# Optimization experiments

Measured on AMD Instinct MI355X. Metric: run time of the kernel, lower is better.

## Reference

```python
import jax, jax.numpy as jnp
import numpy as np
from math import pi

B, L, S, D, H, M, DK, IND, KS = 8, 3072, 3072, 512, 8, 2, 64, 96, 25


def _linear(x, W, b):
    return x @ W + b


def _moving_avg(x, k):
    # Autoformer-style moving average with edge replication, stride 1.  x: [B, T, D]
    pad = (k - 1) // 2
    xp = jnp.concatenate([jnp.repeat(x[:, :1], pad, axis=1), x,
                          jnp.repeat(x[:, -1:], pad, axis=1)], axis=1)
    c = jnp.cumsum(xp, axis=1)
    c = jnp.concatenate([jnp.zeros_like(c[:, :1]), c], axis=1)
    return (c[:, k:] - c[:, :-k]) / k


def _trend_norm(x, g, b):
    # series_decomp(kernel=25): LayerNorm the seasonal part, add back the trend.
    trend = _moving_avg(x, KS)
    seas = x - trend
    mu = jnp.mean(seas, axis=-1, keepdims=True)
    var = jnp.var(seas, axis=-1, keepdims=True)
    return (seas - mu) * jax.lax.rsqrt(var + 1e-5) * g + b + trend


def _quat_attention(q, k, v, q_om, q_th, k_om, k_th):
    # q: [B,Lq,H,E]; k,v: [B,Sk,H,E]; omegas/thetas: [B,*,H,M]
    Bq, Lq, Hh, E = q.shape
    Sk = k.shape[1]
    Mm = q_om.shape[-1]
    qpos = (jnp.arange(Lq, dtype=q.dtype) / Lq)[None, :, None, None]
    kpos = (jnp.arange(Sk, dtype=q.dtype) / Sk)[None, :, None, None]
    Qa = q_om * qpos + q_th
    Ka = k_om * kpos + k_th
    Qc, Qs = jnp.cos(Qa), jnp.sin(Qa)
    Kc, Ks = jnp.cos(Ka), jnp.sin(Ka)
    q0, q1, q2, q3 = jnp.split(q, 4, axis=-1)
    k0, k1, k2, k3 = jnp.split(k, 4, axis=-1)
    op = lambda a, t: jnp.einsum('blhe,blhm->blhme', a, t)
    Qr = jnp.concatenate([op(q0, Qc) - op(q1, Qs), op(q1, Qc) + op(q0, Qs),
                          op(q2, Qc) + op(q3, Qs), op(q3, Qc) - op(q2, Qs)], axis=-1)
    Kr = jnp.concatenate([op(k0, Kc) - op(k2, Ks), op(k1, Kc) - op(k3, Ks),
                          op(k2, Kc) + op(k0, Ks), op(k3, Kc) + op(k1, Ks)], axis=-1)
    scores = jnp.einsum('blhme,bshme->bhls', Qr, Kr) / Mm
    scale = 1.0 / jnp.sqrt(jnp.asarray(E, q.dtype))
    A = jax.nn.softmax(scale * scores, axis=-1)
    return jnp.einsum('bhls,bshd->blhd', A, v)


def _ltr_layer(p, queries, keys, values):
    Bq, Lq, _ = queries.shape
    Sk = keys.shape[1]
    # kernel_size=1 convs == pointwise linears
    q_om = jax.nn.relu(_linear(queries, p['Wqo'], p['bqo'])).reshape(Bq, Lq, H, M)
    k_om = jax.nn.relu(_linear(keys, p['Wko'], p['bko'])).reshape(Bq, Sk, H, M)
    q_th = (jnp.tanh(_linear(queries, p['Wqt'], p['bqt'])) * pi).reshape(Bq, Lq, H, M)
    k_th = (jnp.tanh(_linear(keys, p['Wkt'], p['bkt'])) * pi).reshape(Bq, Sk, H, M)
    q = _linear(queries, p['Wq'], p['bq']).reshape(Bq, Lq, H, DK)
    k = _linear(keys, p['Wk'], p['bk']).reshape(Bq, Sk, H, DK)
    v = _linear(values, p['Wv'], p['bv']).reshape(Bq, Sk, H, DK)
    out = _quat_attention(q, k, v, q_om, q_th, k_om, k_th).reshape(Bq, Lq, H * DK)
    # D-matrix penalty == first-order difference along sequence
    om_pen = jnp.sum(jnp.diff(q_om, axis=1) ** 2) + jnp.sum(jnp.diff(k_om, axis=1) ** 2)
    th_pen = jnp.sum(q_th ** 2) + jnp.sum(k_th ** 2)
    return _linear(out, p['Wo'], p['bo']), om_pen, th_pen


def setup_inputs() -> dict:
    key = jax.random.key(0)
    ks = iter(jax.random.split(key, 32))
    rn = lambda shape, s=1.0: jax.random.normal(next(ks), shape, jnp.float32) * s
    w = 0.03  # ~1/sqrt(d_model)
    return dict(
        queries=rn((B, L, D)), keys=rn((B, S, D)), values=rn((B, S, D)),
        Wq=rn((2, D, D), w), bq=jnp.zeros((2, D), jnp.float32),
        Wk=rn((2, D, D), w), bk=jnp.zeros((2, D), jnp.float32),
        Wv=rn((2, D, D), w), bv=jnp.zeros((2, D), jnp.float32),
        Wqo=rn((2, D, M * H), w), bqo=jnp.zeros((2, M * H), jnp.float32),
        Wko=rn((2, D, M * H), w), bko=jnp.zeros((2, M * H), jnp.float32),
        Wqt=rn((2, D, M * H), w), bqt=jnp.zeros((2, M * H), jnp.float32),
        Wkt=rn((2, D, M * H), w), bkt=jnp.zeros((2, M * H), jnp.float32),
        Wo=rn((2, D, D), w), bo=jnp.zeros((2, D), jnp.float32),
        I=rn((1, IND, D), w),
        ln_g=jnp.ones((D,), jnp.float32), ln_b=jnp.zeros((D,), jnp.float32),
    )


def reference(queries, keys, values, Wq, bq, Wk, bk, Wv, bv, Wqo, bqo, Wko, bko,
              Wqt, bqt, Wkt, bkt, Wo, bo, I, ln_g, ln_b):
    def lp(i):
        return dict(Wq=Wq[i], bq=bq[i], Wk=Wk[i], bk=bk[i], Wv=Wv[i], bv=bv[i],
                    Wqo=Wqo[i], bqo=bqo[i], Wko=Wko[i], bko=bko[i],
                    Wqt=Wqt[i], bqt=bqt[i], Wkt=Wkt[i], bkt=bkt[i],
                    Wo=Wo[i], bo=bo[i])
    Bq = queries.shape[0]
    inducings = jnp.broadcast_to(I, (Bq, IND, D))
    inducings, om1, th1 = _ltr_layer(lp(0), inducings, keys, values)
    inducings = _trend_norm(inducings, ln_g, ln_b)
    out, om2, th2 = _ltr_layer(lp(1), queries, inducings, inducings)
    return out, om1 + om2, th1 + th2
```

## Files before the change

### kernel.cpp

```cpp
#include <hip/hip_runtime.h>
#include <math.h>

#define PI_F 3.14159265358979323846f

namespace {
constexpr int B_ = 8;
constexpr int L_ = 3072;
constexpr int S_ = 3072;
constexpr int H_ = 8;
constexpr int NF = 544;
constexpr int NSC = 8;
constexpr int SCHUNK = S_ / NSC;
}

typedef __attribute__((ext_vector_type(8))) short bf16x8;
typedef __attribute__((ext_vector_type(4))) float f32x4;

__device__ inline f32x4 mfma16(bf16x8 a, bf16x8 b, f32x4 c) {
  return __builtin_amdgcn_mfma_f32_16x16x32_bf16(a, b, c, 0, 0, 0);
}

__device__ inline ushort f2bf(float f) {
  union { float f; unsigned u; } v;
  v.f = f;
  unsigned r = v.u + 0x7FFFu + ((v.u >> 16) & 1u);
  return (ushort)(r >> 16);
}

__device__ inline void gl_lds16(const void* g, void* l) {
  __builtin_amdgcn_global_load_lds(
      (const __attribute__((address_space(1))) unsigned int*)g,
      (__attribute__((address_space(3))) unsigned int*)l, 16, 0, 0);
}

__global__ void init_pen(float* pen) {
  if (threadIdx.x < 16) pen[threadIdx.x] = 0.f;
}

__global__ void write_pen(const float* __restrict__ pen, float* __restrict__ out) {
  if (threadIdx.x == 0) out[12582912] = pen[0];
  if (threadIdx.x == 1) out[12582913] = pen[1];
}

__global__ void pack_w(const float* __restrict__ Wm, const float* __restrict__ Wo_,
                       const float* __restrict__ Wt, const float* __restrict__ bm,
                       const float* __restrict__ bo_, const float* __restrict__ bt,
                       float* __restrict__ Wcat, float* __restrict__ bcat) {
  int gid = blockIdx.x * 256 + threadIdx.x;
  if (gid < 512 * 544) {
    int k = gid / 544, n = gid % 544;
    float v;
    if (n < 512) v = Wm[(size_t)k * 512 + n];
    else if (n < 528) v = Wo_[k * 16 + (n - 512)];
    else v = Wt[k * 16 + (n - 528)];
    Wcat[gid] = v;
  }
  if (gid < 544) {
    float v;
    if (gid < 512) v = bm[gid];
    else if (gid < 528) v = bo_[gid - 512];
    else v = bt[gid - 528];
    bcat[gid] = v;
  }
}

__global__ void pack_wt_fused(const float* __restrict__ Wm, const float* __restrict__ Wo_,
                              const float* __restrict__ Wt, const float* __restrict__ bm,
                              const float* __restrict__ bo_, const float* __restrict__ bt,
                              ushort* __restrict__ BT, float* __restrict__ bias) {
  int gid = blockIdx.x * 256 + threadIdx.x;
  if (gid < 640 * 512) {
    int n = gid >> 9, k = gid & 511;
    float v = 0.f;
    if (n < 512) v = Wm[(size_t)k * 512 + n];
    else if (n < 528) v = Wo_[k * 16 + (n - 512)];
    else if (n < 544) v = Wt[k * 16 + (n - 528)];
    BT[gid] = f2bf(v);
  }
  if (gid < 544)
    bias[gid] = (gid < 512) ? bm[gid] : (gid < 528 ? bo_[gid - 512] : bt[gid - 528]);
}

__global__ void pack_wt_plain(const float* __restrict__ W, const float* __restrict__ b,
                              ushort* __restrict__ BT, float* __restrict__ bias) {
  int gid = blockIdx.x * 256 + threadIdx.x;
  if (gid < 512 * 512) {
    int n = gid >> 9, k = gid & 511;
    BT[gid] = f2bf(W[(size_t)k * 512 + n]);
  }
  if (gid < 512) bias[gid] = b[gid];
}

__global__ __launch_bounds__(256)
void cast_bf16(const float* __restrict__ src, ushort* __restrict__ dst, int n8) {
  int gid = blockIdx.x * 256 + threadIdx.x;
  if (gid < n8) {
    float4 a = ((const float4*)src)[(size_t)gid * 2];
    float4 b = ((const float4*)src)[(size_t)gid * 2 + 1];
    ushort u[8] = {f2bf(a.x), f2bf(a.y), f2bf(a.z), f2bf(a.w),
                   f2bf(b.x), f2bf(b.y), f2bf(b.z), f2bf(b.w)};
    ((uint4*)dst)[gid] = *(uint4*)u;
  }
}

__global__ __launch_bounds__(256)
void gemm_bf16_mfma(const ushort* __restrict__ A, const ushort* __restrict__ BT,
                    const float* __restrict__ bias, float* __restrict__ C,
                    int ldc, int Nout, int act) {
  __shared__ ushort As[128][32];
  __shared__ ushort Bs[128][32];
  const int tid = threadIdx.x;
  const int wv = tid >> 6, lane = tid & 63, quad = lane >> 4, col = lane & 15;
  const int wm = wv & 1, wn = wv >> 1;
  const int m0 = blockIdx.y * 128, n0 = blockIdx.x * 128;

  const int srow = lane >> 2;
  const int scol = (lane & 3) * 8;

  f32x4 acc[4][4];
#pragma unroll
  for (int i = 0; i < 4; ++i)
#pragma unroll
    for (int j = 0; j < 4; ++j) {
      f32x4 z = {0.f, 0.f, 0.f, 0.f};
      acc[i][j] = z;
    }

  const ushort* Ag = A + (size_t)(m0 + wv * 32) * 512;
  const ushort* Bg = BT + (size_t)(n0 + wv * 32) * 512;

  for (int k0 = 0; k0 < 512; k0 += 32) {
    __syncthreads();
    gl_lds16(Ag + (size_t)srow * 512 + k0 + scol, &As[wv * 32][0]);
    gl_lds16(Ag + (size_t)(srow + 16) * 512 + k0 + scol, &As[wv * 32 + 16][0]);
    gl_lds16(Bg + (size_t)srow * 512 + k0 + scol, &Bs[wv * 32][0]);
    gl_lds16(Bg + (size_t)(srow + 16) * 512 + k0 + scol, &Bs[wv * 32 + 16][0]);
    __syncthreads();
    bf16x8 av[4], bv[4];
#pragma unroll
    for (int mi = 0; mi < 4; ++mi)
      av[mi] = *(const bf16x8*)&As[wm * 64 + mi * 16 + col][quad * 8];
#pragma unroll
    for (int ni = 0; ni < 4; ++ni)
      bv[ni] = *(const bf16x8*)&Bs[wn * 64 + ni * 16 + col][quad * 8];
#pragma unroll
    for (int mi = 0; mi < 4; ++mi)
#pragma unroll
      for (int ni = 0; ni < 4; ++ni)
        acc[mi][ni] = mfma16(av[mi], bv[ni], acc[mi][ni]);
  }

#pragma unroll
  for (int mi = 0; mi < 4; ++mi) {
#pragma unroll
    for (int ni = 0; ni < 4; ++ni) {
      int n = n0 + wn * 64 + ni * 16 + col;
      if (n >= Nout) continue;
      float bs = bias[n];
#pragma unroll
      for (int r = 0; r < 4; ++r) {
        int m = m0 + wm * 64 + mi * 16 + quad * 4 + r;
        float v = acc[mi][ni][r] + bs;
        if (act && n >= 512) v = (n < 528) ? fmaxf(v, 0.f) : tanhf(v) * PI_F;
        C[(size_t)m * ldc + n] = v;
      }
    }
  }
}

__global__ __launch_bounds__(256)
void gemm_k512(const float* __restrict__ A, const float* __restrict__ W,
               const float* __restrict__ bias, float* __restrict__ C,
               int M, int N, int act) {
  __shared__ float As[16][68];
  __shared__ float Ws_[16][68];
  const int tid = threadIdx.x;
  const int tx = tid & 15, ty = tid >> 4;
  const int m0 = blockIdx.y * 64, n0 = blockIdx.x * 64;

  float acc[4][4];
#pragma unroll
  for (int i = 0; i < 4; ++i)
#pragma unroll
    for (int j = 0; j < 4; ++j) acc[i][j] = 0.f;

  const int arow = tid >> 2;
  const int acol4 = (tid & 3) * 4;
  const int wrow = tid >> 4;
  const int wcol4 = (tid & 15) * 4;

  for (int k0 = 0; k0 < 512; k0 += 16) {
    float4 av = make_float4(0.f, 0.f, 0.f, 0.f);
    int gm = m0 + arow;
    if (gm < M) av = *(const float4*)(A + (size_t)gm * 512 + k0 + acol4);
    As[acol4 + 0][arow] = av.x;
    As[acol4 + 1][arow] = av.y;
    As[acol4 + 2][arow] = av.z;
    As[acol4 + 3][arow] = av.w;
    float4 wv;
    int gn = n0 + wcol4;
    if (gn + 3 < N) {
      wv = *(const float4*)(W + (size_t)(k0 + wrow) * N + gn);
    } else {
      float tmp[4] = {0.f, 0.f, 0.f, 0.f};
      for (int u = 0; u < 4; ++u)
        if (gn + u < N) tmp[u] = W[(size_t)(k0 + wrow) * N + gn + u];
      wv = make_float4(tmp[0], tmp[1], tmp[2], tmp[3]);
    }
    *(float4*)&Ws_[wrow][wcol4] = wv;
    __syncthreads();
#pragma unroll
    for (int k = 0; k < 16; ++k) {
      float4 a4 = *(const float4*)&As[k][ty * 4];
      float4 b4 = *(const float4*)&Ws_[k][tx * 4];
      float a[4] = {a4.x, a4.y, a4.z, a4.w};
      float b[4] = {b4.x, b4.y, b4.z, b4.w};
#pragma unroll
      for (int i = 0; i < 4; ++i)
#pragma unroll
        for (int j = 0; j < 4; ++j) acc[i][j] = fmaf(a[i], b[j], acc[i][j]);
    }
    __syncthreads();
  }

#pragma unroll
  for (int i = 0; i < 4; ++i) {
    int gm = m0 + ty * 4 + i;
    if (gm >= M) continue;
#pragma unroll
    for (int j = 0; j < 4; ++j) {
      int gn = n0 + tx * 4 + j;
      if (gn >= N) continue;
      float v = acc[i][j] + bias[gn];
      if (act && gn >= 512) v = (gn < 528) ? fmaxf(v, 0.f) : tanhf(v) * PI_F;
      C[(size_t)gm * N + gn] = v;
    }
  }
}

__global__ __launch_bounds__(256)
void build_qr0(const float* __restrict__ QF0, float* __restrict__ Qr0) {
  const int l = blockIdx.x;
  const float* row = QF0 + (size_t)l * NF;
  __shared__ float2 trig[8][2];
  const int tid = threadIdx.x;
  if (tid < 16) {
    int h = tid >> 1, m = tid & 1;
    float om = row[512 + h * 2 + m], th = row[528 + h * 2 + m];
    float qa = fmaf(om, (float)l / 96.f, th);
    trig[h][m] = make_float2(cosf(qa), sinf(qa));
  }
  __syncthreads();
  for (int idx = tid; idx < 1024; idx += 256) {
    int h = idx >> 7, d = idx & 127;
    int m = d >> 6, r = d & 63, c = r >> 4, e = r & 15;
    float qc = row[h * 64 + c * 16 + e];
    float qp = row[h * 64 + (c ^ 1) * 16 + e];
    float2 tg = trig[h][m];
    float sgn = (c == 0 || c == 3) ? -1.f : 1.f;
    Qr0[((size_t)h * 96 + l) * 128 + d] = fmaf(qc, tg.x, sgn * qp * tg.y);
  }
}

__global__ __launch_bounds__(256)
void build_kr1(const float* __restrict__ KF1, float* __restrict__ Kr1) {
  const int rs = blockIdx.x;
  const int b = rs / 96, s = rs % 96;
  const float* row = KF1 + (size_t)rs * NF;
  __shared__ float2 trig[8][2];
  const int tid = threadIdx.x;
  if (tid < 16) {
    int h = tid >> 1, m = tid & 1;
    float om = row[512 + h * 2 + m], th = row[528 + h * 2 + m];
    float ka = fmaf(om, (float)s / 96.f, th);
    trig[h][m] = make_float2(cosf(ka), sinf(ka));
  }
  __syncthreads();
  for (int idx = tid; idx < 1024; idx += 256) {
    int h = idx >> 7, d = idx & 127;
    int m = d >> 6, r = d & 63, c = r >> 4, e = r & 15;
    float kc = row[h * 64 + c * 16 + e];
    float kp = row[h * 64 + (c ^ 2) * 16 + e];
    float2 tg = trig[h][m];
    float sgn = (c < 2) ? -1.f : 1.f;
    Kr1[(((size_t)(b * 8 + h)) * 96 + s) * 128 + d] = fmaf(kc, tg.x, sgn * kp * tg.y);
  }
}

__global__ __launch_bounds__(256)
void attn0_mfma(const float* __restrict__ KF0, const float* __restrict__ V0,
                const float* __restrict__ Qr0, float* __restrict__ accP,
                float* __restrict__ sumP) {
  const int sc = blockIdx.x, h = blockIdx.y, b = blockIdx.z;
  const int tid = threadIdx.x;
  const int wv = tid >> 6, lane = tid & 63, quad = lane >> 4, col = lane & 15;

  __shared__ __align__(16) ushort Qs[96][136];
  __shared__ __align__(16) ushort Ks[64][136];
  __shared__ __align__(16) ushort Vt[64][72];
  __shared__ __align__(16) ushort Ps[96][72];
  __shared__ float rowsum[96];
  __shared__ float2 trig[64][2];

  const float* Qh = Qr0 + ((size_t)h * 96) * 128;
  for (int idx = tid; idx < 96 * 64; idx += 256) {
    int l = idx >> 6, d2 = (idx & 63) * 2;
    float2 q = *(const float2*)(Qh + (size_t)l * 128 + d2);
    ushort2 u;
    u.x = f2bf(q.x);
    u.y = f2bf(q.y);
    *(ushort2*)&Qs[l][d2] = u;
  }
  if (tid < 96) rowsum[tid] = 0.f;

  f32x4 oacc[6];
#pragma unroll
  for (int i = 0; i < 6; ++i) {
    f32x4 z = {0.f, 0.f, 0.f, 0.f};
    oacc[i] = z;
  }

  const int s0g = sc * SCHUNK;
  for (int t = 0; t < 6; ++t) {
    const int sb = s0g + t * 64;
    __syncthreads();
    if (tid < 128) {
      int s = tid >> 1, m = tid & 1;
      const float* row = KF0 + (size_t)(b * S_ + sb + s) * NF;
      float om = row[512 + h * 2 + m];
      float th = row[528 + h * 2 + m];
      float ka = fmaf(om, (float)(sb + s) * (1.f / (float)S_), th);
      trig[s][m] = make_float2(cosf(ka), sinf(ka));
    }
    __syncthreads();
    for (int idx = tid; idx < 64 * 128; idx += 256) {
      int s = idx >> 7, d = idx & 127;
      int m = d >> 6, r = d & 63, c = r >> 4, e = r & 15;
      const float* row = KF0 + (size_t)(b * S_ + sb + s) * NF + h * 64;
      float kc = row[c * 16 + e];
      float kp = row[(c ^ 2) * 16 + e];
      float2 tg = trig[s][m];
      float sgn = (c < 2) ? -1.f : 1.f;
      Ks[s][d] = f2bf(fmaf(kc, tg.x, sgn * kp * tg.y));
    }
    for (int idx = tid; idx < 64 * 64; idx += 256) {
      int s = idx >> 6, d = idx & 63;
      Vt[d][s] = f2bf(V0[(size_t)(b * S_ + sb + s) * 512 + h * 64 + d]);
    }
    __syncthreads();
    bf16x8 bk[4];
#pragma unroll
    for (int k = 0; k < 4; ++k)
      bk[k] = *(const bf16x8*)&Ks[wv * 16 + col][k * 32 + quad * 8];
    f32x4 sacc[6];
#pragma unroll
    for (int mt = 0; mt < 6; ++mt) {
      f32x4 z = {0.f, 0.f, 0.f, 0.f};
      sacc[mt] = z;
#pragma unroll
      for (int k = 0; k < 4; ++k) {
        bf16x8 a = *(const bf16x8*)&Qs[mt * 16 + col][k * 32 + quad * 8];
        sacc[mt] = mfma16(a, bk[k], sacc[mt]);
      }
    }
#pragma unroll
    for (int mt = 0; mt < 6; ++mt) {
      float pr[4];
#pragma unroll
      for (int r = 0; r < 4; ++r) {
        float p = __expf(sacc[mt][r] * 0.0625f);
        pr[r] = p;
        Ps[mt * 16 + quad * 4 + r][wv * 16 + col] = f2bf(p);
      }
#pragma unroll
      for (int r = 0; r < 4; ++r) {
#pragma unroll
        for (int off = 1; off < 16; off <<= 1) pr[r] += __shfl_xor(pr[r], off);
      }
      if (col == 0) {
#pragma unroll
        for (int r = 0; r < 4; ++r)
          atomicAdd(&rowsum[mt * 16 + quad * 4 + r], pr[r]);
      }
    }
    __syncthreads();
    bf16x8 bv0 = *(const bf16x8*)&Vt[wv * 16 + col][quad * 8];
    bf16x8 bv1 = *(const bf16x8*)&Vt[wv * 16 + col][32 + quad * 8];
#pragma unroll
    for (int mt = 0; mt < 6; ++mt) {
      bf16x8 a0 = *(const bf16x8*)&Ps[mt * 16 + col][quad * 8];
      oacc[mt] = mfma16(a0, bv0, oacc[mt]);
      bf16x8 a1 = *(const bf16x8*)&Ps[mt * 16 + col][32 + quad * 8];
      oacc[mt] = mfma16(a1, bv1, oacc[mt]);
    }
  }
  __syncthreads();
  const size_t pbase = (((size_t)(b * 8 + h)) * NSC + sc) * 96;
#pragma unroll
  for (int mt = 0; mt < 6; ++mt) {
#pragma unroll
    for (int r = 0; r < 4; ++r) {
      int l = mt * 16 + quad * 4 + r;
      accP[(pbase + l) * 64 + wv * 16 + col] = oacc[mt][r];
    }
  }
  if (tid < 96) sumP[pbase + tid] = rowsum[tid];
}

__global__ __launch_bounds__(256)
void attn0_stage2(const float* __restrict__ accP, const float* __restrict__ sumP,
                  float* __restrict__ attn0) {
  const int l = blockIdx.x, b = blockIdx.y;
  const int tid = threadIdx.x;
  for (int e = tid; e < 512; e += 256) {
    int h = e >> 6, d = e & 63;
    size_t base = ((size_t)(b * 8 + h)) * NSC * 96;
    float num = 0.f, den = 0.f;
    for (int scv = 0; scv < NSC; ++scv) {
      size_t pb = base + (size_t)scv * 96 + l;
      num += accP[pb * 64 + d];
      den += sumP[pb];
    }
    attn0[((size_t)(b * 96 + l)) * 512 + e] = num / den;
  }
}

__global__ __launch_bounds__(256)
void trend_norm(const float* __restrict__ y, const float* __restrict__ g,
                const float* __restrict__ be, float* __restrict__ outp) {
  const int t = blockIdx.x, b = blockIdx.y;
  const int tid = threadIdx.x;
  __shared__ float red[256];
  __shared__ float red2[256];
  float seas[2], trend[2];
  float lsum = 0.f, lsum2 = 0.f;
#pragma unroll
  for (int u = 0; u < 2; ++u) {
    int d = tid + u * 256;
    float tr = 0.f;
    for (int j = -12; j <= 12; ++j) {
      int tt = t + j;
      tt = tt < 0 ? 0 : (tt > 95 ? 95 : tt);
      tr += y[((size_t)(b * 96 + tt)) * 512 + d];
    }
    tr *= (1.f / 25.f);
    float x = y[((size_t)(b * 96 + t)) * 512 + d];
    float se = x - tr;
    seas[u] = se;
    trend[u] = tr;
    lsum += se;
    lsum2 += se * se;
  }
  red[tid] = lsum;
  red2[tid] = lsum2;
  __syncthreads();
  for (int off = 128; off > 0; off >>= 1) {
    if (tid < off) {
      red[tid] += red[tid + off];
      red2[tid] += red2[tid + off];
    }
    __syncthreads();
  }
  float mu = red[0] / 512.f;
  float var = red2[0] / 512.f - mu * mu;
  float rs = rsqrtf(var + 1e-5f);
#pragma unroll
  for (int u = 0; u < 2; ++u) {
    int d = tid + u * 256;
    outp[((size_t)(b * 96 + t)) * 512 + d] = (seas[u] - mu) * rs * g[d] + be[d] + trend[u];
  }
}

__global__ __launch_bounds__(256)
void penalty(const float* __restrict__ base, int R, int nb, float mult,
             float* __restrict__ pen) {
  const int tid = threadIdx.x;
  size_t gid = (size_t)blockIdx.x * 256 + tid;
  size_t total = (size_t)nb * R * 16;
  float omv = 0.f, thv = 0.f;
  if (gid < total) {
    int j = (int)(gid & 15);
    size_t row = gid >> 4;
    int s = (int)(row % R);
    const float* r0 = base + row * NF;
    float th = r0[528 + j];
    thv = th * th;
    if (s < R - 1) {
      float d = r0[NF + 512 + j] - r0[512 + j];
      omv = d * d;
    }
  }
  __shared__ float ro[256], rt[256];
  ro[tid] = omv;
  rt[tid] = thv;
  __syncthreads();
  for (int off = 128; off > 0; off >>= 1) {
    if (tid < off) {
      ro[tid] += ro[tid + off];
      rt[tid] += rt[tid + off];
    }
    __syncthreads();
  }
  if (tid == 0) {
    atomicAdd(pen + 0, mult * ro[0]);
    atomicAdd(pen + 1, mult * rt[0]);
  }
}

__global__ __launch_bounds__(256)
void attn1_mfma(const float* __restrict__ QF1, const float* __restrict__ Kr1,
                const float* __restrict__ V1, ushort* __restrict__ attn1) {
  const int lt = blockIdx.x, h = blockIdx.y, b = blockIdx.z;
  const int l0 = lt * 64;
  const int tid = threadIdx.x;
  const int wv = tid >> 6, lane = tid & 63, quad = lane >> 4, col = lane & 15;

  __shared__ __align__(16) ushort Qs[64][136];
  __shared__ __align__(16) ushort Ks[96][136];
  __shared__ __align__(16) ushort Vt[64][104];
  __shared__ __align__(16) ushort Ps[64][104];
  __shared__ float2 trigq[64][2];

  if (tid < 128) {
    int l = tid >> 1, m = tid & 1;
    const float* row = QF1 + (size_t)(b * L_ + l0 + l) * NF;
    float om = row[512 + h * 2 + m];
    float th = row[528 + h * 2 + m];
    float qa = fmaf(om, (float)(l0 + l) * (1.f / (float)L_), th);
    trigq[l][m] = make_float2(cosf(qa), sinf(qa));
  }
  __syncthreads();
  for (int idx = tid; idx < 64 * 128; idx += 256) {
    int l = idx >> 7, d = idx & 127;
    int m = d >> 6, r = d & 63, c = r >> 4, e = r & 15;
    const float* row = QF1 + (size_t)(b * L_ + l0 + l) * NF + h * 64;
    float qc = row[c * 16 + e];
    float qp = row[(c ^ 1) * 16 + e];
    float2 tg = trigq[l][m];
    float sgn = (c == 0 || c == 3) ? -1.f : 1.f;
    Qs[l][d] = f2bf(fmaf(qc, tg.x, sgn * qp * tg.y));
  }
  const float* Krb = Kr1 + (size_t)(b * 8 + h) * 96 * 128;
  for (int idx = tid; idx < 96 * 64; idx += 256) {
    int s = idx >> 6, d2 = (idx & 63) * 2;
    float2 kk = *(const float2*)(Krb + (size_t)s * 128 + d2);
    ushort2 u;
    u.x = f2bf(kk.x);
    u.y = f2bf(kk.y);
    *(ushort2*)&Ks[s][d2] = u;
  }
  for (int idx = tid; idx < 96 * 64; idx += 256) {
    int s = idx >> 6, d = idx & 63;
    Vt[d][s] = f2bf(V1[(size_t)(b * 96 + s) * 512 + h * 64 + d]);
  }
  __syncthreads();

  bf16x8 aq[4];
#pragma unroll
  for (int k = 0; k < 4; ++k)
    aq[k] = *(const bf16x8*)&Qs[wv * 16 + col][k * 32 + quad * 8];
  f32x4 sacc[6];
#pragma unroll
  for (int nt = 0; nt < 6; ++nt) {
    f32x4 z = {0.f, 0.f, 0.f, 0.f};
    sacc[nt] = z;
#pragma unroll
    for (int k = 0; k < 4; ++k) {
      bf16x8 bkf = *(const bf16x8*)&Ks[nt * 16 + col][k * 32 + quad * 8];
      sacc[nt] = mfma16(aq[k], bkf, sacc[nt]);
    }
  }
  float rsum[4] = {0.f, 0.f, 0.f, 0.f};
#pragma unroll
  for (int nt = 0; nt < 6; ++nt) {
#pragma unroll
    for (int r = 0; r < 4; ++r) {
      float p = __expf(sacc[nt][r] * 0.0625f);
      Ps[wv * 16 + quad * 4 + r][nt * 16 + col] = f2bf(p);
      rsum[r] += p;
    }
  }
#pragma unroll
  for (int r = 0; r < 4; ++r) {
#pragma unroll
    for (int off = 1; off < 16; off <<= 1) rsum[r] += __shfl_xor(rsum[r], off);
  }
  __syncthreads();
  bf16x8 ap[3];
#pragma unroll
  for (int kt = 0; kt < 3; ++kt)
    ap[kt] = *(const bf16x8*)&Ps[wv * 16 + col][kt * 32 + quad * 8];
  f32x4 oacc[4];
#pragma unroll
  for (int nt = 0; nt < 4; ++nt) {
    f32x4 z = {0.f, 0.f, 0.f, 0.f};
    oacc[nt] = z;
#pragma unroll
    for (int kt = 0; kt < 3; ++kt) {
      bf16x8 bvf = *(const bf16x8*)&Vt[nt * 16 + col][kt * 32 + quad * 8];
      oacc[nt] = mfma16(ap[kt], bvf, oacc[nt]);
    }
  }
  float inv[4];
#pragma unroll
  for (int r = 0; r < 4; ++r) inv[r] = 1.f / rsum[r];
#pragma unroll
  for (int nt = 0; nt < 4; ++nt) {
#pragma unroll
    for (int r = 0; r < 4; ++r) {
      int l = wv * 16 + quad * 4 + r;
      attn1[(size_t)(b * L_ + l0 + l) * 512 + h * 64 + nt * 16 + col] =
          f2bf(oacc[nt][r] * inv[r]);
    }
  }
}

extern "C" void kernel_launch(void* const* d_in, const int* in_sizes, int n_in,
                              void* d_out, int out_size, void* d_ws, size_t ws_size,
                              hipStream_t stream) {
  (void)in_sizes; (void)n_in; (void)out_size; (void)ws_size;
  const float* queries = (const float*)d_in[0];
  const float* keys = (const float*)d_in[1];
  const float* values = (const float*)d_in[2];
  const float* Wq = (const float*)d_in[3];
  const float* bq = (const float*)d_in[4];
  const float* Wk = (const float*)d_in[5];
  const float* bk = (const float*)d_in[6];
  const float* Wv = (const float*)d_in[7];
  const float* bv = (const float*)d_in[8];
  const float* Wqo = (const float*)d_in[9];
  const float* bqo = (const float*)d_in[10];
  const float* Wko = (const float*)d_in[11];
  const float* bko = (const float*)d_in[12];
  const float* Wqt = (const float*)d_in[13];
  const float* bqt = (const float*)d_in[14];
  const float* Wkt = (const float*)d_in[15];
  const float* bkt = (const float*)d_in[16];
  const float* Wo = (const float*)d_in[17];
  const float* bo = (const float*)d_in[18];
  const float* I = (const float*)d_in[19];
  const float* ln_g = (const float*)d_in[20];
  const float* ln_b = (const float*)d_in[21];
  float* out = (float*)d_out;

  float* ws = (float*)d_ws;
  size_t off = 0;
  auto alloc = [&](size_t n) {
    float* p = ws + off;
    off += (n + 3) & ~(size_t)3;
    return p;
  };
  auto allocU = [&](size_t n) { return (ushort*)alloc((n + 1) / 2); };

  float* WCAT0Q = alloc(512 * 544);
  float* WCAT1K = alloc(512 * 544);
  float* BCAT0Q = alloc(544);
  float* BCAT1K = alloc(544);
  ushort* BT0K = allocU(640 * 512);
  ushort* BT1Q = allocU(640 * 512);
  ushort* BTV0 = allocU(512 * 512);
  ushort* BTO1 = allocU(512 * 512);
  float* B0K = alloc(544);
  float* B1Q = alloc(544);
  float* BV0 = alloc(512);
  float* BO1 = alloc(512);
  float* pen = alloc(16);
  float* QF0 = alloc(96 * 544);
  float* Qr0 = alloc(8 * 96 * 128);
  float* KF0 = alloc((size_t)24576 * 544);
  float* V0 = alloc((size_t)24576 * 512);
  float* attn0 = alloc(768 * 512);
  float* y0 = alloc(768 * 512);
  float* xind = alloc(768 * 512);
  float* KF1 = alloc(768 * 544);
  float* V1 = alloc(768 * 512);
  float* Kr1 = alloc((size_t)64 * 96 * 128);
  float* accP = alloc((size_t)64 * NSC * 96 * 64);
  float* sumP = alloc((size_t)64 * NSC * 96);
  ushort* XB1 = allocU((size_t)24576 * 512);
  ushort* XB2 = allocU((size_t)24576 * 512);
  float* QF1 = KF0;

  init_pen<<<1, 64, 0, stream>>>(pen);
  const int packBlocks = (512 * 544 + 255) / 256;
  pack_w<<<packBlocks, 256, 0, stream>>>(Wq, Wqo, Wqt, bq, bqo, bqt, WCAT0Q, BCAT0Q);
  pack_w<<<packBlocks, 256, 0, stream>>>(Wk + 262144, Wko + 8192, Wkt + 8192,
                                         bk + 512, bko + 16, bkt + 16, WCAT1K, BCAT1K);
  pack_wt_fused<<<(640 * 512 + 255) / 256, 256, 0, stream>>>(
      Wk, Wko, Wkt, bk, bko, bkt, BT0K, B0K);
  pack_wt_fused<<<(640 * 512 + 255) / 256, 256, 0, stream>>>(
      Wq + 262144, Wqo + 8192, Wqt + 8192, bq + 512, bqo + 16, bqt + 16, BT1Q, B1Q);
  pack_wt_plain<<<(512 * 512 + 255) / 256, 256, 0, stream>>>(Wv, bv, BTV0, BV0);
  pack_wt_plain<<<(512 * 512 + 255) / 256, 256, 0, stream>>>(Wo + 262144, bo + 512,
                                                             BTO1, BO1);
  const int castBlocks = (24576 * 512 / 8 + 255) / 256;
  cast_bf16<<<castBlocks, 256, 0, stream>>>(keys, XB1, 24576 * 512 / 8);
  cast_bf16<<<castBlocks, 256, 0, stream>>>(values, XB2, 24576 * 512 / 8);

  gemm_bf16_mfma<<<dim3(5, 192), 256, 0, stream>>>(XB1, BT0K, B0K, KF0, 544, 544, 1);
  gemm_bf16_mfma<<<dim3(4, 192), 256, 0, stream>>>(XB2, BTV0, BV0, V0, 512, 512, 0);
  gemm_k512<<<dim3(9, 2), 256, 0, stream>>>(I, WCAT0Q, BCAT0Q, QF0, 96, 544, 1);
  build_qr0<<<96, 256, 0, stream>>>(QF0, Qr0);
  penalty<<<(96 * 16 + 255) / 256, 256, 0, stream>>>(QF0, 96, 1, 8.f, pen);
  penalty<<<(24576 * 16 + 255) / 256, 256, 0, stream>>>(KF0, 3072, 8, 1.f, pen);
  attn0_mfma<<<dim3(8, 8, 8), 256, 0, stream>>>(KF0, V0, Qr0, accP, sumP);
  attn0_stage2<<<dim3(96, 8), 256, 0, stream>>>(accP, sumP, attn0);
  gemm_k512<<<dim3(8, 12), 256, 0, stream>>>(attn0, Wo, bo, y0, 768, 512, 0);
  trend_norm<<<dim3(96, 8), 256, 0, stream>>>(y0, ln_g, ln_b, xind);

  gemm_k512<<<dim3(9, 12), 256, 0, stream>>>(xind, WCAT1K, BCAT1K, KF1, 768, 544, 1);
  gemm_k512<<<dim3(8, 12), 256, 0, stream>>>(xind, Wv + 262144, bv + 512, V1, 768, 512, 0);
  build_kr1<<<768, 256, 0, stream>>>(KF1, Kr1);
  penalty<<<(768 * 16 + 255) / 256, 256, 0, stream>>>(KF1, 96, 8, 1.f, pen);
  cast_bf16<<<castBlocks, 256, 0, stream>>>(queries, XB1, 24576 * 512 / 8);
  gemm_bf16_mfma<<<dim3(5, 192), 256, 0, stream>>>(XB1, BT1Q, B1Q, QF1, 544, 544, 1);
  penalty<<<(24576 * 16 + 255) / 256, 256, 0, stream>>>(QF1, 3072, 8, 1.f, pen);
  attn1_mfma<<<dim3(48, 8, 8), 256, 0, stream>>>(QF1, Kr1, V1, XB2);
  gemm_bf16_mfma<<<dim3(4, 192), 256, 0, stream>>>(XB2, BTO1, BO1, out, 512, 512, 0);
  write_pen<<<1, 64, 0, stream>>>(pen, out);
}
```

Measured before the change: 783.6 us.

## Precompute bf16 rotated Q/K, fuse penalties, batch packing, move small GEMMs to MFMA

Weight packing and input casts are merged into fewer batched launches, and the separate penalty and init kernels are folded into new build_* kernels that also emit rotated Q/K in bf16. The small fp32 GEMMs now use the bf16 MFMA GEMM, which gains M bounds and an optional bf16 output. The attention kernels now read pre-rotated bf16 operands and a transposed V1, and scratch buffers are aliased to cut memory footprint. This aims to reduce launch count, fp32 traffic and redundant trig work inside attention, at the cost of extra intermediate bf16 buffers and more precision loss.

```diff
diff --git a/kernel.cpp b/kernel.cpp
--- a/kernel.cpp
+++ b/kernel.cpp
@@ -7,7 +7,6 @@
 constexpr int B_ = 8;
 constexpr int L_ = 3072;
 constexpr int S_ = 3072;
-constexpr int H_ = 8;
 constexpr int NF = 544;
 constexpr int NSC = 8;
 constexpr int SCHUNK = S_ / NSC;
@@ -33,41 +32,26 @@
       (__attribute__((address_space(3))) unsigned int*)l, 16, 0, 0);
 }
 
-__global__ void init_pen(float* pen) {
-  if (threadIdx.x < 16) pen[threadIdx.x] = 0.f;
-}
-
-__global__ void write_pen(const float* __restrict__ pen, float* __restrict__ out) {
-  if (threadIdx.x == 0) out[12582912] = pen[0];
-  if (threadIdx.x == 1) out[12582913] = pen[1];
-}
-
-__global__ void pack_w(const float* __restrict__ Wm, const float* __restrict__ Wo_,
-                       const float* __restrict__ Wt, const float* __restrict__ bm,
-                       const float* __restrict__ bo_, const float* __restrict__ bt,
-                       float* __restrict__ Wcat, float* __restrict__ bcat) {
-  int gid = blockIdx.x * 256 + threadIdx.x;
-  if (gid < 512 * 544) {
-    int k = gid / 544, n = gid % 544;
-    float v;
-    if (n < 512) v = Wm[(size_t)k * 512 + n];
-    else if (n < 528) v = Wo_[k * 16 + (n - 512)];
-    else v = Wt[k * 16 + (n - 528)];
-    Wcat[gid] = v;
-  }
-  if (gid < 544) {
-    float v;
-    if (gid < 512) v = bm[gid];
-    else if (gid < 528) v = bo_[gid - 512];
-    else v = bt[gid - 528];
-    bcat[gid] = v;
-  }
-}
-
-__global__ void pack_wt_fused(const float* __restrict__ Wm, const float* __restrict__ Wo_,
-                              const float* __restrict__ Wt, const float* __restrict__ bm,
-                              const float* __restrict__ bo_, const float* __restrict__ bt,
-                              ushort* __restrict__ BT, float* __restrict__ bias) {
+__global__ __launch_bounds__(256)
+void pack_fused4(const float* __restrict__ Wq, const float* __restrict__ Wk,
+                 const float* __restrict__ Wqo, const float* __restrict__ Wko,
+                 const float* __restrict__ Wqt, const float* __restrict__ Wkt,
+                 const float* __restrict__ bq, const float* __restrict__ bk,
+                 const float* __restrict__ bqo, const float* __restrict__ bko,
+                 const float* __restrict__ bqt, const float* __restrict__ bkt,
+                 ushort* __restrict__ BTF, float* __restrict__ BF,
+                 float* __restrict__ pen) {
+  const int set = blockIdx.y;
+  const int layer = set >> 1, qs = set & 1;
+  if (blockIdx.x == 0 && set == 0 && threadIdx.x < 16) pen[threadIdx.x] = 0.f;
+  const float* Wm = (qs ? Wq : Wk) + layer * 262144;
+  const float* Wo_ = (qs ? Wqo : Wko) + layer * 8192;
+  const float* Wt = (qs ? Wqt : Wkt) + layer * 8192;
+  const float* bm = (qs ? bq : bk) + layer * 512;
+  const float* bo_ = (qs ? bqo : bko) + layer * 16;
+  const float* bt = (qs ? bqt : bkt) + layer * 16;
+  ushort* BT = BTF + (size_t)set * 640 * 512;
+  float* bias = BF + set * 544;
   int gid = blockIdx.x * 256 + threadIdx.x;
   if (gid < 640 * 512) {
     int n = gid >> 9, k = gid & 511;
@@ -81,8 +65,15 @@
     bias[gid] = (gid < 512) ? bm[gid] : (gid < 528 ? bo_[gid - 512] : bt[gid - 528]);
 }
 
-__global__ void pack_wt_plain(const float* __restrict__ W, const float* __restrict__ b,
-                              ushort* __restrict__ BT, float* __restrict__ bias) {
+__global__ __launch_bounds__(256)
+void pack_plain4(const float* __restrict__ Wv, const float* __restrict__ bv,
+                 const float* __restrict__ Wo, const float* __restrict__ bo,
+                 ushort* __restrict__ BTP, float* __restrict__ BP) {
+  const int set = blockIdx.y;
+  const float* W = (set < 2 ? Wv : Wo) + (set & 1) * 262144;
+  const float* b = (set < 2 ? bv : bo) + (set & 1) * 512;
+  ushort* BT = BTP + (size_t)set * 262144;
+  float* bias = BP + set * 512;
   int gid = blockIdx.x * 256 + threadIdx.x;
   if (gid < 512 * 512) {
     int n = gid >> 9, k = gid & 511;
@@ -91,22 +82,40 @@
   if (gid < 512) bias[gid] = b[gid];
 }
 
-__global__ __launch_bounds__(256)
-void cast_bf16(const float* __restrict__ src, ushort* __restrict__ dst, int n8) {
+__device__ inline void cast8(const float* src, ushort* dst, int i) {
+  float4 a = ((const float4*)src)[(size_t)i * 2];
+  float4 b = ((const float4*)src)[(size_t)i * 2 + 1];
+  ushort u[8] = {f2bf(a.x), f2bf(a.y), f2bf(a.z), f2bf(a.w),
+                 f2bf(b.x), f2bf(b.y), f2bf(b.z), f2bf(b.w)};
+  ((uint4*)dst)[i] = *(uint4*)u;
+}
+
+__global__ __launch_bounds__(256)
+void cast_all(const float* __restrict__ keys, const float* __restrict__ values,
+              const float* __restrict__ I, ushort* __restrict__ keysB,
+              ushort* __restrict__ valuesB, ushort* __restrict__ Ib) {
   int gid = blockIdx.x * 256 + threadIdx.x;
-  if (gid < n8) {
-    float4 a = ((const float4*)src)[(size_t)gid * 2];
-    float4 b = ((const float4*)src)[(size_t)gid * 2 + 1];
-    ushort u[8] = {f2bf(a.x), f2bf(a.y), f2bf(a.z), f2bf(a.w),
-                   f2bf(b.x), f2bf(b.y), f2bf(b.z), f2bf(b.w)};
-    ((uint4*)dst)[gid] = *(uint4*)u;
-  }
+  const int big = 24576 * 512 / 8;
+  if (gid < big) cast8(keys, keysB, gid);
+  else if (gid < 2 * big) cast8(values, valuesB, gid - big);
+  else if (gid < 2 * big + 6144) cast8(I, Ib, gid - 2 * big);
+}
+
+__global__ __launch_bounds__(256)
+void cast_one(const float* __restrict__ src, ushort* __restrict__ dst, int n8) {
+  int gid = blockIdx.x * 256 + threadIdx.x;
+  if (gid < n8) cast8(src, dst, gid);
+}
+
+__global__ void write_pen(const float* __restrict__ pen, float* __restrict__ out) {
+  if (threadIdx.x == 0) out[12582912] = pen[0];
+  if (threadIdx.x == 1) out[12582913] = pen[1];
 }
 
 __global__ __launch_bounds__(256)
 void gemm_bf16_mfma(const ushort* __restrict__ A, const ushort* __restrict__ BT,
-                    const float* __restrict__ bias, float* __restrict__ C,
-                    int ldc, int Nout, int act) {
+                    const float* __restrict__ bias, void* __restrict__ Cv,
+                    int ldc, int M, int Nout, int act, int outBf) {
   __shared__ ushort As[128][32];
   __shared__ ushort Bs[128][32];
   const int tid = threadIdx.x;
@@ -116,6 +125,11 @@
 
   const int srow = lane >> 2;
   const int scol = (lane & 3) * 8;
+  int ar0 = m0 + wv * 32 + srow;
+  int ar1 = ar0 + 16;
+  if (ar0 > M - 1) ar0 = M - 1;
+  if (ar1 > M - 1) ar1 = M - 1;
+  const int br = n0 + wv * 32 + srow;
 
   f32x4 acc[4][4];
 #pragma unroll
@@ -126,15 +140,12 @@
       acc[i][j] = z;
     }
 
-  const ushort* Ag = A + (size_t)(m0 + wv * 32) * 512;
-  const ushort* Bg = BT + (size_t)(n0 + wv * 32) * 512;
-
   for (int k0 = 0; k0 < 512; k0 += 32) {
     __syncthreads();
-    gl_lds16(Ag + (size_t)srow * 512 + k0 + scol, &As[wv * 32][0]);
-    gl_lds16(Ag + (size_t)(srow + 16) * 512 + k0 + scol, &As[wv * 32 + 16][0]);
-    gl_lds16(Bg + (size_t)srow * 512 + k0 + scol, &Bs[wv * 32][0]);
-    gl_lds16(Bg + (size_t)(srow + 16) * 512 + k0 + scol, &Bs[wv * 32 + 16][0]);
+    gl_lds16(A + (size_t)ar0 * 512 + k0 + scol, &As[wv * 32][0]);
+    gl_lds16(A + (size_t)ar1 * 512 + k0 + scol, &As[wv * 32 + 16][0]);
+    gl_lds16(BT + (size_t)br * 512 + k0 + scol, &Bs[wv * 32][0]);
+    gl_lds16(BT + (size_t)(br + 16) * 512 + k0 + scol, &Bs[wv * 32 + 16][0]);
     __syncthreads();
     bf16x8 av[4], bv[4];
 #pragma unroll
@@ -160,86 +171,19 @@
 #pragma unroll
       for (int r = 0; r < 4; ++r) {
         int m = m0 + wm * 64 + mi * 16 + quad * 4 + r;
+        if (m >= M) continue;
         float v = acc[mi][ni][r] + bs;
         if (act && n >= 512) v = (n < 528) ? fmaxf(v, 0.f) : tanhf(v) * PI_F;
-        C[(size_t)m * ldc + n] = v;
-      }
-    }
-  }
-}
-
-__global__ __launch_bounds__(256)
-void gemm_k512(const float* __restrict__ A, const float* __restrict__ W,
-               const float* __restrict__ bias, float* __restrict__ C,
-               int M, int N, int act) {
-  __shared__ float As[16][68];
-  __shared__ float Ws_[16][68];
-  const int tid = threadIdx.x;
-  const int tx = tid & 15, ty = tid >> 4;
-  const int m0 = blockIdx.y * 64, n0 = blockIdx.x * 64;
-
-  float acc[4][4];
-#pragma unroll
-  for (int i = 0; i < 4; ++i)
-#pragma unroll
-    for (int j = 0; j < 4; ++j) acc[i][j] = 0.f;
-
-  const int arow = tid >> 2;
-  const int acol4 = (tid & 3) * 4;
-  const int wrow = tid >> 4;
-  const int wcol4 = (tid & 15) * 4;
-
-  for (int k0 = 0; k0 < 512; k0 += 16) {
-    float4 av = make_float4(0.f, 0.f, 0.f, 0.f);
-    int gm = m0 + arow;
-    if (gm < M) av = *(const float4*)(A + (size_t)gm * 512 + k0 + acol4);
-    As[acol4 + 0][arow] = av.x;
-    As[acol4 + 1][arow] = av.y;
-    As[acol4 + 2][arow] = av.z;
-    As[acol4 + 3][arow] = av.w;
-    float4 wv;
-    int gn = n0 + wcol4;
-    if (gn + 3 < N) {
-      wv = *(const float4*)(W + (size_t)(k0 + wrow) * N + gn);
-    } else {
-      float tmp[4] = {0.f, 0.f, 0.f, 0.f};
-      for (int u = 0; u < 4; ++u)
-        if (gn + u < N) tmp[u] = W[(size_t)(k0 + wrow) * N + gn + u];
-      wv = make_float4(tmp[0], tmp[1], tmp[2], tmp[3]);
-    }
-    *(float4*)&Ws_[wrow][wcol4] = wv;
-    __syncthreads();
-#pragma unroll
-    for (int k = 0; k < 16; ++k) {
-      float4 a4 = *(const float4*)&As[k][ty * 4];
-      float4 b4 = *(const float4*)&Ws_[k][tx * 4];
-      float a[4] = {a4.x, a4.y, a4.z, a4.w};
-      float b[4] = {b4.x, b4.y, b4.z, b4.w};
-#pragma unroll
-      for (int i = 0; i < 4; ++i)
-#pragma unroll
-        for (int j = 0; j < 4; ++j) acc[i][j] = fmaf(a[i], b[j], acc[i][j]);
-    }
-    __syncthreads();
-  }
-
-#pragma unroll
-  for (int i = 0; i < 4; ++i) {
-    int gm = m0 + ty * 4 + i;
-    if (gm >= M) continue;
-#pragma unroll
-    for (int j = 0; j < 4; ++j) {
-      int gn = n0 + tx * 4 + j;
-      if (gn >= N) continue;
-      float v = acc[i][j] + bias[gn];
-      if (act && gn >= 512) v = (gn < 528) ? fmaxf(v, 0.f) : tanhf(v) * PI_F;
-      C[(size_t)gm * N + gn] = v;
-    }
-  }
-}
-
-__global__ __launch_bounds__(256)
-void build_qr0(const float* __restrict__ QF0, float* __restrict__ Qr0) {
+        if (outBf) ((ushort*)Cv)[(size_t)m * ldc + n] = f2bf(v);
+        else ((float*)Cv)[(size_t)m * ldc + n] = v;
+      }
+    }
+  }
+}
+
+__global__ __launch_bounds__(256)
+void build_qr0(const float* __restrict__ QF0, ushort* __restrict__ Qr0bf,
+               float* __restrict__ pen) {
   const int l = blockIdx.x;
   const float* row = QF0 + (size_t)l * NF;
   __shared__ float2 trig[8][2];
@@ -249,6 +193,21 @@
     float om = row[512 + h * 2 + m], th = row[528 + h * 2 + m];
     float qa = fmaf(om, (float)l / 96.f, th);
     trig[h][m] = make_float2(cosf(qa), sinf(qa));
+    float thv = th * th;
+    float omv = 0.f;
+    if (l < 95) {
+      float d = QF0[(size_t)(l + 1) * NF + 512 + tid] - row[512 + tid];
+      omv = d * d;
+    }
+#pragma unroll
+    for (int off = 1; off < 16; off <<= 1) {
+      omv += __shfl_xor(omv, off);
+      thv += __shfl_xor(thv, off);
+    }
+    if (tid == 0) {
+      atomicAdd(pen + 0, 8.f * omv);
+      atomicAdd(pen + 1, 8.f * thv);
+    }
   }
   __syncthreads();
   for (int idx = tid; idx < 1024; idx += 256) {
@@ -258,12 +217,103 @@
     float qp = row[h * 64 + (c ^ 1) * 16 + e];
     float2 tg = trig[h][m];
     float sgn = (c == 0 || c == 3) ? -1.f : 1.f;
-    Qr0[((size_t)h * 96 + l) * 128 + d] = fmaf(qc, tg.x, sgn * qp * tg.y);
-  }
-}
-
-__global__ __launch_bounds__(256)
-void build_kr1(const float* __restrict__ KF1, float* __restrict__ Kr1) {
+    Qr0bf[((size_t)h * 96 + l) * 128 + d] = f2bf(fmaf(qc, tg.x, sgn * qp * tg.y));
+  }
+}
+
+__global__ __launch_bounds__(256)
+void build_kr0(const float* __restrict__ KF0, ushort* __restrict__ Kr0bf,
+               float* __restrict__ pen) {
+  const int st = blockIdx.x, h = blockIdx.y, b = blockIdx.z;
+  const int s0 = st * 64;
+  const int tid = threadIdx.x;
+  __shared__ float2 trig[64][2];
+  if (tid < 128) {
+    int s = tid >> 1, m = tid & 1;
+    int sg = s0 + s;
+    const float* row = KF0 + (size_t)(b * S_ + sg) * NF;
+    float om = row[512 + h * 2 + m];
+    float th = row[528 + h * 2 + m];
+    float ka = fmaf(om, (float)sg * (1.f / (float)S_), th);
+    trig[s][m] = make_float2(cosf(ka), sinf(ka));
+    float thv = th * th;
+    float omv = 0.f;
+    if (sg < S_ - 1) {
+      float d = KF0[(size_t)(b * S_ + sg + 1) * NF + 512 + h * 2 + m] - om;
+      omv = d * d;
+    }
+#pragma unroll
+    for (int off = 1; off < 64; off <<= 1) {
+      omv += __shfl_xor(omv, off);
+      thv += __shfl_xor(thv, off);
+    }
+    if ((tid & 63) == 0) {
+      atomicAdd(pen + 0, omv);
+      atomicAdd(pen + 1, thv);
+    }
+  }
+  __syncthreads();
+  ushort* outb = Kr0bf + ((size_t)(b * 8 + h) * S_ + s0) * 128;
+  for (int idx = tid; idx < 64 * 128; idx += 256) {
+    int s = idx >> 7, d = idx & 127;
+    int m = d >> 6, r = d & 63, c = r >> 4, e = r & 15;
+    const float* rowh = KF0 + (size_t)(b * S_ + s0 + s) * NF + h * 64;
+    float kc = rowh[c * 16 + e];
+    float kp = rowh[(c ^ 2) * 16 + e];
+    float2 tg = trig[s][m];
+    float sgn = (c < 2) ? -1.f : 1.f;
+    outb[(size_t)s * 128 + d] = f2bf(fmaf(kc, tg.x, sgn * kp * tg.y));
+  }
+}
+
+__global__ __launch_bounds__(256)
+void build_qr1(const float* __restrict__ QF1, ushort* __restrict__ Qr1bf,
+               float* __restrict__ pen) {
+  const int st = blockIdx.x, h = blockIdx.y, b = blockIdx.z;
+  const int l0 = st * 64;
+  const int tid = threadIdx.x;
+  __shared__ float2 trig[64][2];
+  if (tid < 128) {
+    int l = tid >> 1, m = tid & 1;
+    int lg = l0 + l;
+    const float* row = QF1 + (size_t)(b * L_ + lg) * NF;
+    float om = row[512 + h * 2 + m];
+    float th = row[528 + h * 2 + m];
+    float qa = fmaf(om, (float)lg * (1.f / (float)L_), th);
+    trig[l][m] = make_float2(cosf(qa), sinf(qa));
+    float thv = th * th;
+    float omv = 0.f;
+    if (lg < L_ - 1) {
+      float d = QF1[(size_t)(b * L_ + lg + 1) * NF + 512 + h * 2 + m] - om;
+      omv = d * d;
+    }
+#pragma unroll
+    for (int off = 1; off < 64; off <<= 1) {
+      omv += __shfl_xor(omv, off);
+      thv += __shfl_xor(thv, off);
+    }
+    if ((tid & 63) == 0) {
+      atomicAdd(pen + 0, omv);
+      atomicAdd(pen + 1, thv);
+    }
+  }
+  __syncthreads();
+  ushort* outb = Qr1bf + ((size_t)(b * 8 + h) * L_ + l0) * 128;
+  for (int idx = tid; idx < 64 * 128; idx += 256) {
+    int l = idx >> 7, d = idx & 127;
+    int m = d >> 6, r = d & 63, c = r >> 4, e = r & 15;
+    const float* rowh = QF1 + (size_t)(b * L_ + l0 + l) * NF + h * 64;
+    float qc = rowh[c * 16 + e];
+    float qp = rowh[(c ^ 1) * 16 + e];
+    float2 tg = trig[l][m];
+    float sgn = (c == 0 || c == 3) ? -1.f : 1.f;
+    outb[(size_t)l * 128 + d] = f2bf(fmaf(qc, tg.x, sgn * qp * tg.y));
+  }
+}
+
+__global__ __launch_bounds__(256)
+void build_kr1(const float* __restrict__ KF1, ushort* __restrict__ Kr1bf,
+               float* __restrict__ pen) {
   const int rs = blockIdx.x;
   const int b = rs / 96, s = rs % 96;
   const float* row = KF1 + (size_t)rs * NF;
@@ -274,6 +324,21 @@
     float om = row[512 + h * 2 + m], th = row[528 + h * 2 + m];
     float ka = fmaf(om, (float)s / 96.f, th);
     trig[h][m] = make_float2(cosf(ka), sinf(ka));
+    float thv = th * th;
+    float omv = 0.f;
+    if (s < 95) {
+      float d = KF1[(size_t)(rs + 1) * NF + 512 + tid] - row[512 + tid];
+      omv = d * d;
+    }
+#pragma unroll
+    for (int off = 1; off < 16; off <<= 1) {
+      omv += __shfl_xor(omv, off);
+      thv += __shfl_xor(thv, off);
+    }
+    if (tid == 0) {
+      atomicAdd(pen + 0, omv);
+      atomicAdd(pen + 1, thv);
+    }
   }
   __syncthreads();
   for (int idx = tid; idx < 1024; idx += 256) {
@@ -283,13 +348,24 @@
     float kp = row[h * 64 + (c ^ 2) * 16 + e];
     float2 tg = trig[h][m];
     float sgn = (c < 2) ? -1.f : 1.f;
-    Kr1[(((size_t)(b * 8 + h)) * 96 + s) * 128 + d] = fmaf(kc, tg.x, sgn * kp * tg.y);
-  }
-}
-
-__global__ __launch_bounds__(256)
-void attn0_mfma(const float* __restrict__ KF0, const float* __restrict__ V0,
-                const float* __restrict__ Qr0, float* __restrict__ accP,
+    Kr1bf[(((size_t)(b * 8 + h)) * 96 + s) * 128 + d] = f2bf(fmaf(kc, tg.x, sgn * kp * tg.y));
+  }
+}
+
+__global__ __launch_bounds__(256)
+void build_v1t(const float* __restrict__ V1, ushort* __restrict__ V1T) {
+  const int h = blockIdx.x, b = blockIdx.y;
+  const int tid = threadIdx.x;
+  for (int idx = tid; idx < 6144; idx += 256) {
+    int s = idx >> 6, d = idx & 63;
+    float v = V1[(size_t)(b * 96 + s) * 512 + h * 64 + d];
+    V1T[((size_t)(b * 8 + h) * 64 + d) * 96 + s] = f2bf(v);
+  }
+}
+
+__global__ __launch_bounds__(256)
+void attn0_mfma(const ushort* __restrict__ Kr0bf, const ushort* __restrict__ V0bf,
+                const ushort* __restrict__ Qr0bf, float* __restrict__ accP,
                 float* __restrict__ sumP) {
   const int sc = blockIdx.x, h = blockIdx.y, b = blockIdx.z;
   const int tid = threadIdx.x;
@@ -300,16 +376,14 @@
   __shared__ __align__(16) ushort Vt[64][72];
   __shared__ __align__(16) ushort Ps[96][72];
   __shared__ float rowsum[96];
-  __shared__ float2 trig[64][2];
-
-  const float* Qh = Qr0 + ((size_t)h * 96) * 128;
-  for (int idx = tid; idx < 96 * 64; idx += 256) {
-    int l = idx >> 6, d2 = (idx & 63) * 2;
-    float2 q = *(const float2*)(Qh + (size_t)l * 128 + d2);
-    ushort2 u;
-    u.x = f2bf(q.x);
-    u.y = f2bf(q.y);
-    *(ushort2*)&Qs[l][d2] = u;
+
+  {
+    const ushort* src = Qr0bf + (size_t)h * 96 * 128;
+    for (int idx = tid; idx < 1536; idx += 256) {
+      int row = idx >> 4, g = idx & 15;
+      uint4 v = *(const uint4*)(src + (size_t)row * 128 + g * 8);
+      *(uint4*)&Qs[row][g * 8] = v;
+    }
   }
   if (tid < 96) rowsum[tid] = 0.f;
 
@@ -321,31 +395,18 @@
   }
 
   const int s0g = sc * SCHUNK;
+  const ushort* Krb = Kr0bf + (size_t)(b * 8 + h) * S_ * 128;
   for (int t = 0; t < 6; ++t) {
     const int sb = s0g + t * 64;
     __syncthreads();
-    if (tid < 128) {
-      int s = tid >> 1, m = tid & 1;
-      const float* row = KF0 + (size_t)(b * S_ + sb + s) * NF;
-      float om = row[512 + h * 2 + m];
-      float th = row[528 + h * 2 + m];
-      float ka = fmaf(om, (float)(sb + s) * (1.f / (float)S_), th);
-      trig[s][m] = make_float2(cosf(ka), sinf(ka));
-    }
-    __syncthreads();
-    for (int idx = tid; idx < 64 * 128; idx += 256) {
-      int s = idx >> 7, d = idx & 127;
-      int m = d >> 6, r = d & 63, c = r >> 4, e = r & 15;
-      const float* row = KF0 + (size_t)(b * S_ + sb + s) * NF + h * 64;
-      float kc = row[c * 16 + e];
-      float kp = row[(c ^ 2) * 16 + e];
-      float2 tg = trig[s][m];
-      float sgn = (c < 2) ? -1.f : 1.f;
-      Ks[s][d] = f2bf(fmaf(kc, tg.x, sgn * kp * tg.y));
-    }
-    for (int idx = tid; idx < 64 * 64; idx += 256) {
+    for (int idx = tid; idx < 1024; idx += 256) {
+      int row = idx >> 4, g = idx & 15;
+      uint4 v = *(const uint4*)(Krb + (size_t)(sb + row) * 128 + g * 8);
+      *(uint4*)&Ks[row][g * 8] = v;
+    }
+    for (int idx = tid; idx < 4096; idx += 256) {
       int s = idx >> 6, d = idx & 63;
-      Vt[d][s] = f2bf(V0[(size_t)(b * S_ + sb + s) * 512 + h * 64 + d]);
+      Vt[d][s] = V0bf[(size_t)(b * S_ + sb + s) * 512 + h * 64 + d];
     }
     __syncthreads();
     bf16x8 bk[4];
@@ -409,7 +470,7 @@
 
 __global__ __launch_bounds__(256)
 void attn0_stage2(const float* __restrict__ accP, const float* __restrict__ sumP,
-                  float* __restrict__ attn0) {
+                  ushort* __restrict__ attn0B) {
   const int l = blockIdx.x, b = blockIdx.y;
   const int tid = threadIdx.x;
   for (int e = tid; e < 512; e += 256) {
@@ -421,13 +482,13 @@
       num += accP[pb * 64 + d];
       den += sumP[pb];
     }
-    attn0[((size_t)(b * 96 + l)) * 512 + e] = num / den;
+    attn0B[((size_t)(b * 96 + l)) * 512 + e] = f2bf(num / den);
   }
 }
 
 __global__ __launch_bounds__(256)
 void trend_norm(const float* __restrict__ y, const float* __restrict__ g,
-                const float* __restrict__ be, float* __restrict__ outp) {
+                const float* __restrict__ be, ushort* __restrict__ outp) {
   const int t = blockIdx.x, b = blockIdx.y;
   const int tid = threadIdx.x;
   __shared__ float red[256];
@@ -467,51 +528,15 @@
 #pragma unroll
   for (int u = 0; u < 2; ++u) {
     int d = tid + u * 256;
-    outp[((size_t)(b * 96 + t)) * 512 + d] = (seas[u] - mu) * rs * g[d] + be[d] + trend[u];
-  }
-}
-
-__global__ __launch_bounds__(256)
-void penalty(const float* __restrict__ base, int R, int nb, float mult,
-             float* __restrict__ pen) {
-  const int tid = threadIdx.x;
-  size_t gid = (size_t)blockIdx.x * 256 + tid;
-  size_t total = (size_t)nb * R * 16;
-  float omv = 0.f, thv = 0.f;
-  if (gid < total) {
-    int j = (int)(gid & 15);
-    size_t row = gid >> 4;
-    int s = (int)(row % R);
-    const float* r0 = base + row * NF;
-    float th = r0[528 + j];
-    thv = th * th;
-    if (s < R - 1) {
-      float d = r0[NF + 512 + j] - r0[512 + j];
-      omv = d * d;
-    }
-  }
-  __shared__ float ro[256], rt[256];
-  ro[tid] = omv;
-  rt[tid] = thv;
-  __syncthreads();
-  for (int off = 128; off > 0; off >>= 1) {
-    if (tid < off) {
-      ro[tid] += ro[tid + off];
-      rt[tid] += rt[tid + off];
-    }
-    __syncthreads();
-  }
-  if (tid == 0) {
-    atomicAdd(pen + 0, mult * ro[0]);
-    atomicAdd(pen + 1, mult * rt[0]);
-  }
-}
-
-__global__ __launch_bounds__(256)
-void attn1_mfma(const float* __restrict__ QF1, const float* __restrict__ Kr1,
-                const float* __restrict__ V1, ushort* __restrict__ attn1) {
-  const int lt = blockIdx.x, h = blockIdx.y, b = blockIdx.z;
-  const int l0 = lt * 64;
+    outp[((size_t)(b * 96 + t)) * 512 + d] =
+        f2bf((seas[u] - mu) * rs * g[d] + be[d] + trend[u]);
+  }
+}
+
+__global__ __launch_bounds__(256)
+void attn1_mfma(const ushort* __restrict__ Qr1bf, const ushort* __restrict__ Kr1bf,
+                const ushort* __restrict__ V1T, ushort* __restrict__ attn1B) {
+  const int lg = blockIdx.x, h = blockIdx.y, b = blockIdx.z;
   const int tid = threadIdx.x;
   const int wv = tid >> 6, lane = tid & 63, quad = lane >> 4, col = lane & 15;
 
@@ -519,98 +544,89 @@
   __shared__ __align__(16) ushort Ks[96][136];
   __shared__ __align__(16) ushort Vt[64][104];
   __shared__ __align__(16) ushort Ps[64][104];
-  __shared__ float2 trigq[64][2];
-
-  if (tid < 128) {
-    int l = tid >> 1, m = tid & 1;
-    const float* row = QF1 + (size_t)(b * L_ + l0 + l) * NF;
-    float om = row[512 + h * 2 + m];
-    float th = row[528 + h * 2 + m];
-    float qa = fmaf(om, (float)(l0 + l) * (1.f / (float)L_), th);
-    trigq[l][m] = make_float2(cosf(qa), sinf(qa));
+
+  {
+    const ushort* src = Kr1bf + (size_t)(b * 8 + h) * 96 * 128;
+    for (int idx = tid; idx < 1536; idx += 256) {
+      int row = idx >> 4, g = idx & 15;
+      uint4 v = *(const uint4*)(src + (size_t)row * 128 + g * 8);
+      *(uint4*)&Ks[row][g * 8] = v;
+    }
+    const ushort* vsrc = V1T + (size_t)(b * 8 + h) * 64 * 96;
+    for (int idx = tid; idx < 768; idx += 256) {
+      int row = idx / 12, g = idx % 12;
+      uint4 v = *(const uint4*)(vsrc + (size_t)row * 96 + g * 8);
+      *(uint4*)&Vt[row][g * 8] = v;
+    }
   }
   __syncthreads();
-  for (int idx = tid; idx < 64 * 128; idx += 256) {
-    int l = idx >> 7, d = idx & 127;
-    int m = d >> 6, r = d & 63, c = r >> 4, e = r & 15;
-    const float* row = QF1 + (size_t)(b * L_ + l0 + l) * NF + h * 64;
-    float qc = row[c * 16 + e];
-    float qp = row[(c ^ 1) * 16 + e];
-    float2 tg = trigq[l][m];
-    float sgn = (c == 0 || c == 3) ? -1.f : 1.f;
-    Qs[l][d] = f2bf(fmaf(qc, tg.x, sgn * qp * tg.y));
-  }
-  const float* Krb = Kr1 + (size_t)(b * 8 + h) * 96 * 128;
-  for (int idx = tid; idx < 96 * 64; idx += 256) {
-    int s = idx >> 6, d2 = (idx & 63) * 2;
-    float2 kk = *(const float2*)(Krb + (size_t)s * 128 + d2);
-    ushort2 u;
-    u.x = f2bf(kk.x);
-    u.y = f2bf(kk.y);
-    *(ushort2*)&Ks[s][d2] = u;
-  }
-  for (int idx = tid; idx < 96 * 64; idx += 256) {
-    int s = idx >> 6, d = idx & 63;
-    Vt[d][s] = f2bf(V1[(size_t)(b * 96 + s) * 512 + h * 64 + d]);
-  }
-  __syncthreads();
-
-  bf16x8 aq[4];
-#pragma unroll
-  for (int k = 0; k < 4; ++k)
-    aq[k] = *(const bf16x8*)&Qs[wv * 16 + col][k * 32 + quad * 8];
-  f32x4 sacc[6];
-#pragma unroll
-  for (int nt = 0; nt < 6; ++nt) {
-    f32x4 z = {0.f, 0.f, 0.f, 0.f};
-    sacc[nt] = z;
-#pragma unroll
-    for (int k = 0; k < 4; ++k) {
-      bf16x8 bkf = *(const bf16x8*)&Ks[nt * 16 + col][k * 32 + quad * 8];
-      sacc[nt] = mfma16(aq[k], bkf, sacc[nt]);
-    }
-  }
-  float rsum[4] = {0.f, 0.f, 0.f, 0.f};
-#pragma unroll
-  for (int nt = 0; nt < 6; ++nt) {
+
+  const ushort* qbase = Qr1bf + (size_t)(b * 8 + h) * L_ * 128;
+  for (int lt = 0; lt < 4; ++lt) {
+    const int l0 = (lg * 4 + lt) * 64;
+    for (int idx = tid; idx < 1024; idx += 256) {
+      int row = idx >> 4, g = idx & 15;
+      uint4 v = *(const uint4*)(qbase + (size_t)(l0 + row) * 128 + g * 8);
+      *(uint4*)&Qs[row][g * 8] = v;
+    }
+    __syncthreads();
+    bf16x8 aq[4];
+#pragma unroll
+    for (int k = 0; k < 4; ++k)
+      aq[k] = *(const bf16x8*)&Qs[wv * 16 + col][k * 32 + quad * 8];
+    f32x4 sacc[6];
+#pragma unroll
+    for (int nt = 0; nt < 6; ++nt) {
+      f32x4 z = {0.f, 0.f, 0.f, 0.f};
+      sacc[nt] = z;
+#pragma unroll
+      for (int k = 0; k < 4; ++k) {
+        bf16x8 bkf = *(const bf16x8*)&Ks[nt * 16 + col][k * 32 + quad * 8];
+        sacc[nt] = mfma16(aq[k], bkf, sacc[nt]);
+      }
+    }
+    float rsum[4] = {0.f, 0.f, 0.f, 0.f};
+#pragma unroll
+    for (int nt = 0; nt < 6; ++nt) {
+#pragma unroll
+      for (int r = 0; r < 4; ++r) {
+        float p = __expf(sacc[nt][r] * 0.0625f);
+        Ps[wv * 16 + quad * 4 + r][nt * 16 + col] = f2bf(p);
+        rsum[r] += p;
+      }
+    }
 #pragma unroll
     for (int r = 0; r < 4; ++r) {
-      float p = __expf(sacc[nt][r] * 0.0625f);
-      Ps[wv * 16 + quad * 4 + r][nt * 16 + col] = f2bf(p);
-      rsum[r] += p;
-    }
-  }
-#pragma unroll
-  for (int r = 0; r < 4; ++r) {
-#pragma unroll
-    for (int off = 1; off < 16; off <<= 1) rsum[r] += __shfl_xor(rsum[r], off);
-  }
-  __syncthreads();
-  bf16x8 ap[3];
-#pragma unroll
-  for (int kt = 0; kt < 3; ++kt)
-    ap[kt] = *(const bf16x8*)&Ps[wv * 16 + col][kt * 32 + quad * 8];
-  f32x4 oacc[4];
-#pragma unroll
-  for (int nt = 0; nt < 4; ++nt) {
-    f32x4 z = {0.f, 0.f, 0.f, 0.f};
-    oacc[nt] = z;
-#pragma unroll
-    for (int kt = 0; kt < 3; ++kt) {
-      bf16x8 bvf = *(const bf16x8*)&Vt[nt * 16 + col][kt * 32 + quad * 8];
-      oacc[nt] = mfma16(ap[kt], bvf, oacc[nt]);
-    }
-  }
-  float inv[4];
-#pragma unroll
-  for (int r = 0; r < 4; ++r) inv[r] = 1.f / rsum[r];
-#pragma unroll
-  for (int nt = 0; nt < 4; ++nt) {
-#pragma unroll
-    for (int r = 0; r < 4; ++r) {
-      int l = wv * 16 + quad * 4 + r;
-      attn1[(size_t)(b * L_ + l0 + l) * 512 + h * 64 + nt * 16 + col] =
-          f2bf(oacc[nt][r] * inv[r]);
+#pragma unroll
+      for (int off = 1; off < 16; off <<= 1) rsum[r] += __shfl_xor(rsum[r], off);
+    }
+    __syncthreads();
+    bf16x8 ap[3];
+#pragma unroll
+    for (int kt = 0; kt < 3; ++kt)
+      ap[kt] = *(const bf16x8*)&Ps[wv * 16 + col][kt * 32 + quad * 8];
+    f32x4 oacc[4];
+#pragma unroll
+    for (int nt = 0; nt < 4; ++nt) {
+      f32x4 z = {0.f, 0.f, 0.f, 0.f};
+      oacc[nt] = z;
+#pragma unroll
+      for (int kt = 0; kt < 3; ++kt) {
+        bf16x8 bvf = *(const bf16x8*)&Vt[nt * 16 + col][kt * 32 + quad * 8];
+        oacc[nt] = mfma16(ap[kt], bvf, oacc[nt]);
+      }
+    }
+    float inv[4];
+#pragma unroll
+    for (int r = 0; r < 4; ++r) inv[r] = 1.f / rsum[r];
+#pragma unroll
+    for (int nt = 0; nt < 4; ++nt) {
+#pragma unroll
+      for (int r = 0; r < 4; ++r) {
+        int l = wv * 16 + quad * 4 + r;
+        attn1B[(size_t)(b * L_ + l0 + l) * 512 + h * 64 + nt * 16 + col] =
+            f2bf(oacc[nt][r] * inv[r]);
+      }
     }
   }
 }
@@ -652,70 +668,91 @@
   };
   auto allocU = [&](size_t n) { return (ushort*)alloc((n + 1) / 2); };
 
-  float* WCAT0Q = alloc(512 * 544);
-  float* WCAT1K = alloc(512 * 544);
-  float* BCAT0Q = alloc(544);
-  float* BCAT1K = alloc(544);
-  ushort* BT0K = allocU(640 * 512);
-  ushort* BT1Q = allocU(640 * 512);
-  ushort* BTV0 = allocU(512 * 512);
-  ushort* BTO1 = allocU(512 * 512);
-  float* B0K = alloc(544);
-  float* B1Q = alloc(544);
-  float* BV0 = alloc(512);
-  float* BO1 = alloc(512);
+  ushort* BTF = allocU((size_t)4 * 640 * 512);
+  float* BF = alloc(4 * 544);
+  ushort* BTP = allocU((size_t)4 * 512 * 512);
+  float* BP = alloc(4 * 512);
   float* pen = alloc(16);
+  ushort* keysB = allocU((size_t)24576 * 512);
+  ushort* valuesB = allocU((size_t)24576 * 512);
+  ushort* Ib = allocU(96 * 512);
   float* QF0 = alloc(96 * 544);
-  float* Qr0 = alloc(8 * 96 * 128);
+  ushort* Qr0bf = allocU(8 * 96 * 128);
   float* KF0 = alloc((size_t)24576 * 544);
-  float* V0 = alloc((size_t)24576 * 512);
-  float* attn0 = alloc(768 * 512);
-  float* y0 = alloc(768 * 512);
-  float* xind = alloc(768 * 512);
-  float* KF1 = alloc(768 * 544);
-  float* V1 = alloc(768 * 512);
-  float* Kr1 = alloc((size_t)64 * 96 * 128);
-  float* accP = alloc((size_t)64 * NSC * 96 * 64);
-  float* sumP = alloc((size_t)64 * NSC * 96);
-  ushort* XB1 = allocU((size_t)24576 * 512);
-  ushort* XB2 = allocU((size_t)24576 * 512);
+  ushort* V0bf = allocU((size_t)24576 * 512);
+  ushort* Kr0bf = allocU((size_t)64 * 3072 * 128);
+
+  float* sb = (float*)keysB;
+  size_t soff = 0;
+  auto salloc = [&](size_t n) {
+    float* p = sb + soff;
+    soff += (n + 3) & ~(size_t)3;
+    return p;
+  };
+  float* accP = salloc((size_t)64 * NSC * 96 * 64);
+  float* sumP = salloc((size_t)64 * NSC * 96);
+  ushort* attn0B = (ushort*)salloc(768 * 512 / 2);
+  float* y0 = salloc(768 * 512);
+  ushort* xindB = (ushort*)salloc(768 * 512 / 2);
+  float* KF1 = salloc(768 * 544);
+  float* V1 = salloc(768 * 512);
+  ushort* Kr1bf = (ushort*)salloc((size_t)64 * 96 * 128 / 2);
+  ushort* V1T = (ushort*)salloc((size_t)64 * 64 * 96 / 2);
+
+  ushort* queriesB = valuesB;
   float* QF1 = KF0;
-
-  init_pen<<<1, 64, 0, stream>>>(pen);
-  const int packBlocks = (512 * 544 + 255) / 256;
-  pack_w<<<packBlocks, 256, 0, stream>>>(Wq, Wqo, Wqt, bq, bqo, bqt, WCAT0Q, BCAT0Q);
-  pack_w<<<packBlocks, 256, 0, stream>>>(Wk + 262144, Wko + 8192, Wkt + 8192,
-                                         bk + 512, bko + 16, bkt + 16, WCAT1K, BCAT1K);
-  pack_wt_fused<<<(640 * 512 + 255) / 256, 256, 0, stream>>>(
-      Wk, Wko, Wkt, bk, bko, bkt, BT0K, B0K);
-  pack_wt_fused<<<(640 * 512 + 255) / 256, 256, 0, stream>>>(
-      Wq + 262144, Wqo + 8192, Wqt + 8192, bq + 512, bqo + 16, bqt + 16, BT1Q, B1Q);
-  pack_wt_plain<<<(512 * 512 + 255) / 256, 256, 0, stream>>>(Wv, bv, BTV0, BV0);
-  pack_wt_plain<<<(512 * 512 + 255) / 256, 256, 0, stream>>>(Wo + 262144, bo + 512,
-                                                             BTO1, BO1);
-  const int castBlocks = (24576 * 512 / 8 + 255) / 256;
-  cast_bf16<<<castBlocks, 256, 0, stream>>>(keys, XB1, 24576 * 512 / 8);
-  cast_bf16<<<castBlocks, 256, 0, stream>>>(values, XB2, 24576 * 512 / 8);
-
-  gemm_bf16_mfma<<<dim3(5, 192), 256, 0, stream>>>(XB1, BT0K, B0K, KF0, 544, 544, 1);
-  gemm_bf16_mfma<<<dim3(4, 192), 256, 0, stream>>>(XB2, BTV0, BV0, V0, 512, 512, 0);
-  gemm_k512<<<dim3(9, 2), 256, 0, stream>>>(I, WCAT0Q, BCAT0Q, QF0, 96, 544, 1);
-  build_qr0<<<96, 256, 0, stream>>>(QF0, Qr0);
-  penalty<<<(96 * 16 + 255) / 256, 256, 0, stream>>>(QF0, 96, 1, 8.f, pen);
-  penalty<<<(24576 * 16 + 255) / 256, 256, 0, stream>>>(KF0, 3072, 8, 1.f, pen);
-  attn0_mfma<<<dim3(8, 8, 8), 256, 0, stream>>>(KF0, V0, Qr0, accP, sumP);
-  attn0_stage2<<<dim3(96, 8), 256, 0, stream>>>(accP, sumP, attn0);
-  gemm_k512<<<dim3(8, 12), 256, 0, stream>>>(attn0, Wo, bo, y0, 768, 512, 0);
-  trend_norm<<<dim3(96, 8), 256, 0, stream>>>(y0, ln_g, ln_b, xind);
-
-  gemm_k512<<<dim3(9, 12), 256, 0, stream>>>(xind, WCAT1K, BCAT1K, KF1, 768, 544, 1);
-  gemm_k512<<<dim3(8, 12), 256, 0, stream>>>(xind, Wv + 262144, bv + 512, V1, 768, 512, 0);
-  build_kr1<<<768, 256, 0, stream>>>(KF1, Kr1);
-  penalty<<<(768 * 16 + 255) / 256, 256, 0, stream>>>(KF1, 96, 8, 1.f, pen);
-  cast_bf16<<<castBlocks, 256, 0, stream>>>(queries, XB1, 24576 * 512 / 8);
-  gemm_bf16_mfma<<<dim3(5, 192), 256, 0, stream>>>(XB1, BT1Q, B1Q, QF1, 544, 544, 1);
-  penalty<<<(24576 * 16 + 255) / 256, 256, 0, stream>>>(QF1, 3072, 8, 1.f, pen);
-  attn1_mfma<<<dim3(48, 8, 8), 256, 0, stream>>>(QF1, Kr1, V1, XB2);
-  gemm_bf16_mfma<<<dim3(4, 192), 256, 0, stream>>>(XB2, BTO1, BO1, out, 512, 512, 0);
+  ushort* Qr1bf = Kr0bf;
+  ushort* attn1B = V0bf;
+
+  ushort* BT0K = BTF;
+  ushort* BT0Q = BTF + 327680;
+  ushort* BT1K = BTF + 2 * 327680;
+  ushort* BT1Q = BTF + 3 * 327680;
+  float* B0K = BF;
+  float* B0Q = BF + 544;
+  float* B1K = BF + 1088;
+  float* B1Q = BF + 1632;
+  ushort* BTV0 = BTP;
+  ushort* BTV1 = BTP + 262144;
+  ushort* BTO0 = BTP + 2 * 262144;
+  ushort* BTO1 = BTP + 3 * 262144;
+  float* BV0 = BP;
+  float* BV1 = BP + 512;
+  float* BO0 = BP + 1024;
+  float* BO1 = BP + 1536;
+
+  pack_fused4<<<dim3(1280, 4), 256, 0, stream>>>(Wq, Wk, Wqo, Wko, Wqt, Wkt, bq, bk,
+                                                 bqo, bko, bqt, bkt, BTF, BF, pen);
+  pack_plain4<<<dim3(1024, 4), 256, 0, stream>>>(Wv, bv, Wo, bo, BTP, BP);
+  cast_all<<<(2 * 1572864 + 6144 + 255) / 256, 256, 0, stream>>>(keys, values, I,
+                                                                 keysB, valuesB, Ib);
+
+  gemm_bf16_mfma<<<dim3(5, 192), 256, 0, stream>>>(keysB, BT0K, B0K, KF0, 544,
+                                                   24576, 544, 1, 0);
+  gemm_bf16_mfma<<<dim3(4, 192), 256, 0, stream>>>(valuesB, BTV0, BV0, V0bf, 512,
+                                                   24576, 512, 0, 1);
+  gemm_bf16_mfma<<<dim3(5, 1), 256, 0, stream>>>(Ib, BT0Q, B0Q, QF0, 544,
+                                                 96, 544, 1, 0);
+  build_qr0<<<96, 256, 0, stream>>>(QF0, Qr0bf, pen);
+  build_kr0<<<dim3(48, 8, 8), 256, 0, stream>>>(KF0, Kr0bf, pen);
+  attn0_mfma<<<dim3(8, 8, 8), 256, 0, stream>>>(Kr0bf, V0bf, Qr0bf, accP, sumP);
+  attn0_stage2<<<dim3(96, 8), 256, 0, stream>>>(accP, sumP, attn0B);
+  gemm_bf16_mfma<<<dim3(4, 6), 256, 0, stream>>>(attn0B, BTO0, BO0, y0, 512,
+                                                 768, 512, 0, 0);
+  trend_norm<<<dim3(96, 8), 256, 0, stream>>>(y0, ln_g, ln_b, xindB);
+
+  gemm_bf16_mfma<<<dim3(5, 6), 256, 0, stream>>>(xindB, BT1K, B1K, KF1, 544,
+                                                 768, 544, 1, 0);
+  gemm_bf16_mfma<<<dim3(4, 6), 256, 0, stream>>>(xindB, BTV1, BV1, V1, 512,
+                                                 768, 512, 0, 0);
+  build_kr1<<<768, 256, 0, stream>>>(KF1, Kr1bf, pen);
+  build_v1t<<<dim3(8, 8), 256, 0, stream>>>(V1, V1T);
+  cast_one<<<6144, 256, 0, stream>>>(queries, queriesB, 1572864);
+  gemm_bf16_mfma<<<dim3(5, 192), 256, 0, stream>>>(queriesB, BT1Q, B1Q, QF1, 544,
+                                                   24576, 544, 1, 0);
+  build_qr1<<<dim3(48, 8, 8), 256, 0, stream>>>(QF1, Qr1bf, pen);
+  attn1_mfma<<<dim3(12, 8, 8), 256, 0, stream>>>(Qr1bf, Kr1bf, V1T, attn1B);
+  gemm_bf16_mfma<<<dim3(4, 192), 256, 0, stream>>>(attn1B, BTO1, BO1, out, 512,
+                                                   24576, 512, 0, 0);
   write_pen<<<1, 64, 0, stream>>>(pen, out);
 }
```

After: 955.0 us. 21.9% more time.
